# Optimization experiments

Hardware: AMD Instinct MI355X
Metric: run time of the kernel (lower is better)

Reference implementation:

```python
import jax, jax.numpy as jnp
import numpy as np

B, L, D, K, MAXL = 2, 1024, 256, 64, 1024
EPS = 1e-5

def _encode(x, pos, w1, b1, w2, b2, wa, ba):
    # x: [B,L,D] -> complex phasors [B,L,K]
    xa = x + pos[: x.shape[1]][None]
    h = jax.nn.gelu(xa @ w1 + b1, approximate=False)
    phase = jnp.tanh(h @ w2 + b2) * np.float32(np.pi)
    amp = jax.nn.softplus(xa @ wa + ba) + np.float32(0.1)
    return (amp * jnp.exp(1j * phase)).astype(jnp.complex64)

def setup_inputs() -> dict:
    key = jax.random.key(0)
    ks = jax.random.split(key, 24)
    def lin_w(k, i, o):
        return (jax.random.normal(k, (i, o), jnp.float32) / np.sqrt(np.float32(i)))
    def pos(k):
        return jax.random.normal(k, (MAXL, D), jnp.float32) * np.float32(0.02)
    inp = {
        'x': jax.random.normal(ks[0], (B, L, D), jnp.float32),
        'pos_k': pos(ks[1]),
        'w1_k': lin_w(ks[2], D, D), 'b1_k': jnp.zeros((D,), jnp.float32),
        'w2_k': lin_w(ks[3], D, K), 'b2_k': jnp.zeros((K,), jnp.float32),
        'wa_k': lin_w(ks[4], D, K), 'ba_k': jnp.zeros((K,), jnp.float32),
        'pos_q': pos(ks[5]),
        'w1_q': lin_w(ks[6], D, D), 'b1_q': jnp.zeros((D,), jnp.float32),
        'w2_q': lin_w(ks[7], D, K), 'b2_q': jnp.zeros((K,), jnp.float32),
        'wa_q': lin_w(ks[8], D, K), 'ba_q': jnp.zeros((K,), jnp.float32),
        'wv': lin_w(ks[9], D, D), 'bv': jnp.zeros((D,), jnp.float32),
        'ln_g': jnp.ones((D,), jnp.float32), 'ln_b': jnp.zeros((D,), jnp.float32),
        'wo': lin_w(ks[10], D, D), 'bo': jnp.zeros((D,), jnp.float32),
    }
    return inp

def reference(x, pos_k, w1_k, b1_k, w2_k, b2_k, wa_k, ba_k,
              pos_q, w1_q, b1_q, w2_q, b2_q, wa_q, ba_q,
              wv, bv, ln_g, ln_b, wo, bo):
    Bx, Lx, Dx = x.shape
    kp = _encode(x, pos_k, w1_k, b1_k, w2_k, b2_k, wa_k, ba_k)  # [B,L,K] complex
    qp = _encode(x, pos_q, w1_q, b1_q, w2_q, b2_q, wa_q, ba_q)  # [B,L,K] complex
    V = (x @ wv + bv).astype(jnp.complex64)                      # [B,L,D]
    bound = kp[:, :, :, None] * V[:, :, None, :]                 # [B,L,K,D]
    memory = jnp.cumsum(bound, axis=1)                           # [B,L,K,D]
    retrieved = jnp.real(jnp.einsum('blkd,blk->bld', memory, jnp.conj(qp)))
    positions = jnp.arange(1, Lx + 1, dtype=jnp.float32)
    norm = jnp.sqrt(positions * np.float32(kp.shape[-1]))[None, :, None]
    r = retrieved / norm
    mu = jnp.mean(r, axis=-1, keepdims=True)
    var = jnp.var(r, axis=-1, keepdims=True)
    rn = (r - mu) / jnp.sqrt(var + np.float32(EPS)) * ln_g + ln_b
    return x + rn @ wo + bo
```

## Files before the change

kernel.cpp:

```cpp
#include <hip/hip_runtime.h>
#include <hip/hip_bf16.h>

typedef __attribute__((ext_vector_type(8))) short short8;
typedef __attribute__((ext_vector_type(4))) float float4v;

constexpr int B = 2, L = 1024, D = 256, K = 64;
constexpr int N = B * L;
constexpr int NC = L / 64;
constexpr int TM_CSTRIDE = 2 * K * D;
constexpr int TM_BSTRIDE = NC * TM_CSTRIDE;

constexpr int WT2_OFF = 393216;

__device__ __forceinline__ ushort bf16_hi(float v) {
  return (ushort)(__float_as_uint(v) >> 16);
}
__device__ __forceinline__ float hi_f(float v) {
  return __uint_as_float(__float_as_uint(v) & 0xFFFF0000u);
}
__device__ __forceinline__ ushort bf16_rne(float v) {
  uint b = __float_as_uint(v);
  b += 0x7FFF + ((b >> 16) & 1);
  return (ushort)(b >> 16);
}

__global__ __launch_bounds__(256) void prep_kernel(
    const float* __restrict__ w1_k, const float* __restrict__ w1_q,
    const float* __restrict__ wv,
    const float* __restrict__ w2_k, const float* __restrict__ wa_k,
    const float* __restrict__ w2_q, const float* __restrict__ wa_q,
    ushort* __restrict__ WT) {
  __shared__ float Lt[64][65];
  const int bi = blockIdx.x, tid = threadIdx.x;
  const float* src;
  int ncols, k0, n0;
  ushort* dhi;
  int losz;
  if (bi < 48) {
    const int m = bi >> 4, t = bi & 15;
    src = (m == 0) ? w1_k : (m == 1) ? w1_q : wv;
    ncols = 256; k0 = (t >> 2) * 64; n0 = (t & 3) * 64;
    dhi = WT + m * 131072; losz = 65536;
  } else {
    const int m = (bi - 48) >> 2, kt = (bi - 48) & 3;
    src = (m == 0) ? w2_k : (m == 1) ? wa_k : (m == 2) ? w2_q : wa_q;
    ncols = 64; k0 = kt * 64; n0 = 0;
    dhi = WT + WT2_OFF + m * 32768; losz = 16384;
  }
  ushort* dlo = dhi + losz;
  for (int p = 0; p < 16; ++p) {
    const int kr = p * 4 + (tid >> 6), nc = tid & 63;
    Lt[kr][nc] = src[(k0 + kr) * ncols + n0 + nc];
  }
  __syncthreads();
  const int n = tid >> 2, kq = tid & 3;
  uint uh[8], ul[8];
  for (int i = 0; i < 8; ++i) {
    const float v0 = Lt[kq * 16 + 2 * i][n];
    const float v1 = Lt[kq * 16 + 2 * i + 1][n];
    uh[i] = (uint)bf16_hi(v0) | ((uint)bf16_hi(v1) << 16);
    ul[i] = (uint)bf16_rne(v0 - hi_f(v0)) | ((uint)bf16_rne(v1 - hi_f(v1)) << 16);
  }
  const int oidx = (n0 + n) * 256 + k0 + kq * 16;
  *(uint4*)&dhi[oidx] = make_uint4(uh[0], uh[1], uh[2], uh[3]);
  *(uint4*)&dhi[oidx + 8] = make_uint4(uh[4], uh[5], uh[6], uh[7]);
  *(uint4*)&dlo[oidx] = make_uint4(ul[0], ul[1], ul[2], ul[3]);
  *(uint4*)&dlo[oidx + 8] = make_uint4(ul[4], ul[5], ul[6], ul[7]);
}

__global__ __launch_bounds__(256) void enc1_kernel(
    const float* __restrict__ x, const float* __restrict__ pos_k,
    const float* __restrict__ pos_q,
    const float* __restrict__ b1_k, const float* __restrict__ b1_q,
    const float* __restrict__ bv, const ushort* __restrict__ WT,
    float* __restrict__ hk, float* __restrict__ hq, float* __restrict__ V) {
  __shared__ __align__(16) ushort Ah[32][40], Al[32][40];
  __shared__ __align__(16) ushort Bh[128][40], Bl[128][40];
  const int tid = threadIdx.x;
  const int g = blockIdx.x / 128;
  const int rem = blockIdx.x % 128;
  const int row0 = (rem >> 1) * 32, nb = (rem & 1) * 128;
  const float* pos = (g == 0) ? pos_k : (g == 1) ? pos_q : nullptr;
  const ushort* Wh = WT + g * 131072;
  const ushort* Wl = Wh + 65536;
  const int w = tid >> 6, lane = tid & 63;
  const int m16 = lane & 15, quad = lane >> 4;

  float4v acc[2][2] = {};

  for (int k0 = 0; k0 < 256; k0 += 32) {
    __syncthreads();
    {
      const int r = tid >> 3, kc = (tid & 7) * 4;
      const int row = row0 + r, l = row & (L - 1);
      float4 xv = *(const float4*)&x[row * D + k0 + kc];
      if (pos) {
        const float4 pv = *(const float4*)&pos[l * D + k0 + kc];
        xv.x += pv.x; xv.y += pv.y; xv.z += pv.z; xv.w += pv.w;
      }
      ushort4 h4, l4;
      h4.x = bf16_hi(xv.x); l4.x = bf16_rne(xv.x - hi_f(xv.x));
      h4.y = bf16_hi(xv.y); l4.y = bf16_rne(xv.y - hi_f(xv.y));
      h4.z = bf16_hi(xv.z); l4.z = bf16_rne(xv.z - hi_f(xv.z));
      h4.w = bf16_hi(xv.w); l4.w = bf16_rne(xv.w - hi_f(xv.w));
      *(ushort4*)&Ah[r][kc] = h4;
      *(ushort4*)&Al[r][kc] = l4;
    }
#pragma unroll
    for (int p = 0; p < 2; ++p) {
      const int n = (tid >> 2) + p * 64, chunk = tid & 3;
      const int ga = (nb + n) * 256 + k0 + chunk * 8;
      *(uint4*)&Bh[n][chunk * 8] = *(const uint4*)&Wh[ga];
      *(uint4*)&Bl[n][chunk * 8] = *(const uint4*)&Wl[ga];
    }
    __syncthreads();

    short8 afh[2], afl[2], bfh[2], bfl[2];
#pragma unroll
    for (int r = 0; r < 2; ++r) {
      afh[r] = *(const short8*)&Ah[r * 16 + m16][quad * 8];
      afl[r] = *(const short8*)&Al[r * 16 + m16][quad * 8];
    }
#pragma unroll
    for (int c = 0; c < 2; ++c) {
      const int col = w * 32 + c * 16 + m16;
      bfh[c] = *(const short8*)&Bh[col][quad * 8];
      bfl[c] = *(const short8*)&Bl[col][quad * 8];
    }
#pragma unroll
    for (int r = 0; r < 2; ++r)
#pragma unroll
      for (int c = 0; c < 2; ++c) {
        acc[r][c] = __builtin_amdgcn_mfma_f32_16x16x32_bf16(afh[r], bfh[c], acc[r][c], 0, 0, 0);
        acc[r][c] = __builtin_amdgcn_mfma_f32_16x16x32_bf16(afh[r], bfl[c], acc[r][c], 0, 0, 0);
        acc[r][c] = __builtin_amdgcn_mfma_f32_16x16x32_bf16(afl[r], bfh[c], acc[r][c], 0, 0, 0);
      }
  }

  float* outp = (g == 0) ? hk : (g == 1) ? hq : V;
  const float* bp = (g == 0) ? b1_k : (g == 1) ? b1_q : bv;
#pragma unroll
  for (int c = 0; c < 2; ++c) {
    const int colg = nb + w * 32 + c * 16 + m16;
    const float bias = bp[colg];
#pragma unroll
    for (int r = 0; r < 2; ++r)
#pragma unroll
      for (int j = 0; j < 4; ++j) {
        const int rowg = row0 + r * 16 + quad * 4 + j;
        float v = acc[r][c][j] + bias;
        if (g < 2) v = 0.5f * v * (1.0f + erff(v * 0.70710678f));
        outp[rowg * D + colg] = v;
      }
  }
}

__global__ __launch_bounds__(256) void enc2_kernel(
    const float* __restrict__ x, const float* __restrict__ pos_k,
    const float* __restrict__ pos_q, const float* __restrict__ hk,
    const float* __restrict__ hq,
    const float* __restrict__ b2_k, const float* __restrict__ ba_k,
    const float* __restrict__ b2_q, const float* __restrict__ ba_q,
    const ushort* __restrict__ WT,
    float* __restrict__ kr, float* __restrict__ ki,
    float* __restrict__ qr, float* __restrict__ qi) {
  __shared__ __align__(16) ushort Ahh[16][40], Ahl[16][40], Axh[16][40], Axl[16][40];
  __shared__ __align__(16) ushort B2h[64][40], B2l[64][40], Bah[64][40], Bal[64][40];
  const int tid = threadIdx.x;
  const int e = blockIdx.x >> 7;
  const int r0g = (blockIdx.x & 127) * 16;
  const float* hsrc = e ? hq : hk;
  const float* pos = e ? pos_q : pos_k;
  const ushort* W2h = WT + WT2_OFF + (e ? 2 : 0) * 32768;
  const ushort* W2l = W2h + 16384;
  const ushort* Wah = WT + WT2_OFF + (e ? 3 : 1) * 32768;
  const ushort* Wal = Wah + 16384;
  const int w = tid >> 6, lane = tid & 63;
  const int m16 = lane & 15, quad = lane >> 4;

  float4v accP = {}, accA = {};
  for (int k0 = 0; k0 < 256; k0 += 32) {
    __syncthreads();
    {
      const int r = tid >> 4, kc = (tid & 15) * 2;
      const int row = r0g + r, l = row & (L - 1);
      const float2 hv = *(const float2*)&hsrc[row * D + k0 + kc];
      const float2 xv = *(const float2*)&x[row * D + k0 + kc];
      const float2 pv = *(const float2*)&pos[l * D + k0 + kc];
      const float a0 = xv.x + pv.x, a1 = xv.y + pv.y;
      ushort2 t;
      t.x = bf16_hi(hv.x); t.y = bf16_hi(hv.y); *(ushort2*)&Ahh[r][kc] = t;
      t.x = bf16_rne(hv.x - hi_f(hv.x)); t.y = bf16_rne(hv.y - hi_f(hv.y));
      *(ushort2*)&Ahl[r][kc] = t;
      t.x = bf16_hi(a0); t.y = bf16_hi(a1); *(ushort2*)&Axh[r][kc] = t;
      t.x = bf16_rne(a0 - hi_f(a0)); t.y = bf16_rne(a1 - hi_f(a1));
      *(ushort2*)&Axl[r][kc] = t;
    }
    {
      const int n = tid >> 2, chunk = tid & 3;
      const int ga = n * 256 + k0 + chunk * 8;
      *(uint4*)&B2h[n][chunk * 8] = *(const uint4*)&W2h[ga];
      *(uint4*)&B2l[n][chunk * 8] = *(const uint4*)&W2l[ga];
      *(uint4*)&Bah[n][chunk * 8] = *(const uint4*)&Wah[ga];
      *(uint4*)&Bal[n][chunk * 8] = *(const uint4*)&Wal[ga];
    }
    __syncthreads();

    const short8 ahh = *(const short8*)&Ahh[m16][quad * 8];
    const short8 ahl = *(const short8*)&Ahl[m16][quad * 8];
    const short8 axh = *(const short8*)&Axh[m16][quad * 8];
    const short8 axl = *(const short8*)&Axl[m16][quad * 8];
    const int col = w * 16 + m16;
    const short8 b2h = *(const short8*)&B2h[col][quad * 8];
    const short8 b2l = *(const short8*)&B2l[col][quad * 8];
    const short8 bah = *(const short8*)&Bah[col][quad * 8];
    const short8 bal = *(const short8*)&Bal[col][quad * 8];
    accP = __builtin_amdgcn_mfma_f32_16x16x32_bf16(ahh, b2h, accP, 0, 0, 0);
    accP = __builtin_amdgcn_mfma_f32_16x16x32_bf16(ahh, b2l, accP, 0, 0, 0);
    accP = __builtin_amdgcn_mfma_f32_16x16x32_bf16(ahl, b2h, accP, 0, 0, 0);
    accA = __builtin_amdgcn_mfma_f32_16x16x32_bf16(axh, bah, accA, 0, 0, 0);
    accA = __builtin_amdgcn_mfma_f32_16x16x32_bf16(axh, bal, accA, 0, 0, 0);
    accA = __builtin_amdgcn_mfma_f32_16x16x32_bf16(axl, bah, accA, 0, 0, 0);
  }

  float* pr = e ? qr : kr;
  float* pim = e ? qi : ki;
  const float* b2 = e ? b2_q : b2_k;
  const float* ba = e ? ba_q : ba_k;
  const int colk = w * 16 + m16;
  const float b2v = b2[colk], bav = ba[colk];
#pragma unroll
  for (int j = 0; j < 4; ++j) {
    const int row = r0g + quad * 4 + j;
    const float ph = tanhf(accP[j] + b2v) * 3.14159265358979f;
    const float av = accA[j] + bav;
    const float am = fmaxf(av, 0.0f) + log1pf(expf(-fabsf(av))) + 0.1f;
    pr[row * K + colk] = am * cosf(ph);
    pim[row * K + colk] = am * sinf(ph);
  }
}

__global__ __launch_bounds__(256) void tbuild_kernel(
    const float* __restrict__ kr, const float* __restrict__ ki,
    const float* __restrict__ V, float* __restrict__ TM) {
  const int id = blockIdx.x;
  const int dc = id & 15, c = (id >> 4) & 15, b = id >> 8;
  const int tid = threadIdx.x;
  const int n0 = b * L + c * 64;
  const int d = dc * 16 + (tid & 15);
  const int kb = tid >> 4;

  __shared__ float krL[64][68], kiL[64][68];
  for (int e = tid; e < 1024; e += 256) {
    const int t = e >> 4, k4 = (e & 15) * 4;
    *(float4*)&krL[t][k4] = *(const float4*)&kr[(n0 + t) * K + k4];
    *(float4*)&kiL[t][k4] = *(const float4*)&ki[(n0 + t) * K + k4];
  }
  __syncthreads();

  float vcol[64];
#pragma unroll 8
  for (int t = 0; t < 64; ++t) vcol[t] = V[(n0 + t) * D + d];

  float ar[4] = {0.f, 0.f, 0.f, 0.f}, ai[4] = {0.f, 0.f, 0.f, 0.f};
#pragma unroll 4
  for (int t = 0; t < 64; ++t) {
    const float vt = vcol[t];
    const float4 k4r = *(const float4*)&krL[t][kb * 4];
    const float4 k4i = *(const float4*)&kiL[t][kb * 4];
    ar[0] += k4r.x * vt; ar[1] += k4r.y * vt; ar[2] += k4r.z * vt; ar[3] += k4r.w * vt;
    ai[0] += k4i.x * vt; ai[1] += k4i.y * vt; ai[2] += k4i.z * vt; ai[3] += k4i.w * vt;
  }

  const size_t base = (size_t)b * TM_BSTRIDE + (size_t)c * TM_CSTRIDE;
#pragma unroll
  for (int i = 0; i < 4; ++i) {
    const int k = kb * 4 + i;
    TM[base + (size_t)k * D + d] = ar[i];
    TM[base + (size_t)(K + k) * D + d] = ai[i];
  }
}

__global__ __launch_bounds__(256) void scan_kernel(float* __restrict__ TM) {
  const int col = blockIdx.x * 256 + threadIdx.x;
  const int d = col & 255;
  const int k = (col >> 8) & 63;
  const int comp = (col >> 14) & 1;
  const int b = col >> 15;
  size_t idx = (size_t)b * TM_BSTRIDE + (size_t)comp * (K * D) + (size_t)k * D + d;
  float run = 0.f;
#pragma unroll
  for (int c = 0; c < NC; ++c, idx += TM_CSTRIDE) {
    const float t = TM[idx];
    TM[idx] = run;
    run += t;
  }
}

__global__ __launch_bounds__(256) void out_kernel(
    const float* __restrict__ qr, const float* __restrict__ qi,
    const float* __restrict__ kr, const float* __restrict__ ki,
    const float* __restrict__ V, const float* __restrict__ TM,
    const float* __restrict__ x,
    const float* __restrict__ ln_g, const float* __restrict__ ln_b,
    const float* __restrict__ wo, const float* __restrict__ bo,
    float* __restrict__ out) {
  const int tid = threadIdx.x;
  const int r0 = blockIdx.x * 2;
  const int b = r0 >> 10;
  const int l0 = r0 & (L - 1);
  const int c = l0 >> 6;
  const int lo = l0 & 63;
  const int n0 = b * L + c * 64;
  const int nrows = lo + 2;

  __shared__ float qrL[2][K], qiL[2][K];
  __shared__ float krL[64][68], kiL[64][68];
  __shared__ float SL[2][64];
  __shared__ float rn[2][D];
  __shared__ float red[2][2][4];

  if (tid < 128) {
    const int r = tid >> 6, k = tid & 63;
    qrL[r][k] = qr[(r0 + r) * K + k];
    qiL[r][k] = qi[(r0 + r) * K + k];
  }
  for (int e = tid; e < nrows * 16; e += 256) {
    const int t = e >> 4, k4 = (e & 15) * 4;
    *(float4*)&krL[t][k4] = *(const float4*)&kr[(n0 + t) * K + k4];
    *(float4*)&kiL[t][k4] = *(const float4*)&ki[(n0 + t) * K + k4];
  }
  __syncthreads();

  if (tid < 128) {
    const int rq = tid >> 6, t = tid & 63;
    float s = 0.f;
    if (t <= lo + rq) {
#pragma unroll
      for (int k4 = 0; k4 < K; k4 += 4) {
        const float4 a = *(const float4*)&qrL[rq][k4];
        const float4 bb = *(const float4*)&qiL[rq][k4];
        const float4 kk = *(const float4*)&krL[t][k4];
        const float4 kki = *(const float4*)&kiL[t][k4];
        s += a.x * kk.x + a.y * kk.y + a.z * kk.z + a.w * kk.w +
             bb.x * kki.x + bb.y * kki.y + bb.z * kki.z + bb.w * kki.w;
      }
    }
    SL[rq][t] = s;
  }
  __syncthreads();

  float acc0 = 0.f, acc1 = 0.f;
  const float* Mr = TM + (size_t)b * TM_BSTRIDE + (size_t)c * TM_CSTRIDE;
  const float* Mi = Mr + K * D;
  for (int k4 = 0; k4 < K; k4 += 4) {
    const float4 q0r = *(const float4*)&qrL[0][k4];
    const float4 q0i = *(const float4*)&qiL[0][k4];
    const float4 q1r = *(const float4*)&qrL[1][k4];
    const float4 q1i = *(const float4*)&qiL[1][k4];
#pragma unroll
    for (int j = 0; j < 4; ++j) {
      const float mr = Mr[(size_t)(k4 + j) * D + tid];
      const float mi = Mi[(size_t)(k4 + j) * D + tid];
      acc0 += ((const float*)&q0r)[j] * mr + ((const float*)&q0i)[j] * mi;
      acc1 += ((const float*)&q1r)[j] * mr + ((const float*)&q1i)[j] * mi;
    }
  }
  {
    const int tmax = lo + 1;
    for (int t = 0; t <= tmax; ++t) {
      const float vt = V[(n0 + t) * D + tid];
      acc0 += SL[0][t] * vt;
      acc1 += SL[1][t] * vt;
    }
  }

  float val[2];
  val[0] = acc0 * rsqrtf((float)(l0 + 1) * 64.0f);
  val[1] = acc1 * rsqrtf((float)(l0 + 2) * 64.0f);
  const int w = tid >> 6;
#pragma unroll
  for (int rq = 0; rq < 2; ++rq) {
    float v = val[rq], v2 = v * v;
    for (int off = 32; off > 0; off >>= 1) {
      v += __shfl_xor(v, off, 64);
      v2 += __shfl_xor(v2, off, 64);
    }
    if ((tid & 63) == 0) { red[rq][0][w] = v; red[rq][1][w] = v2; }
  }
  __syncthreads();

  const float g = ln_g[tid], bb = ln_b[tid];
#pragma unroll
  for (int rq = 0; rq < 2; ++rq) {
    const float s = red[rq][0][0] + red[rq][0][1] + red[rq][0][2] + red[rq][0][3];
    const float sq = red[rq][1][0] + red[rq][1][1] + red[rq][1][2] + red[rq][1][3];
    const float mu = s * (1.0f / 256.0f);
    const float var = sq * (1.0f / 256.0f) - mu * mu;
    rn[rq][tid] = (val[rq] - mu) * rsqrtf(var + 1e-5f) * g + bb;
  }
  __syncthreads();

  float ao0, ao1;
  ao0 = ao1 = bo[tid];
  for (int d4 = 0; d4 < D; d4 += 4) {
    float wj[4];
#pragma unroll
    for (int j = 0; j < 4; ++j) wj[j] = wo[(d4 + j) * D + tid];
    const float4 r0v = *(const float4*)&rn[0][d4];
    const float4 r1v = *(const float4*)&rn[1][d4];
    ao0 += r0v.x * wj[0] + r0v.y * wj[1] + r0v.z * wj[2] + r0v.w * wj[3];
    ao1 += r1v.x * wj[0] + r1v.y * wj[1] + r1v.z * wj[2] + r1v.w * wj[3];
  }
  out[(r0 + 0) * D + tid] = x[(r0 + 0) * D + tid] + ao0;
  out[(r0 + 1) * D + tid] = x[(r0 + 1) * D + tid] + ao1;
}

extern "C" void kernel_launch(void* const* d_in, const int* in_sizes, int n_in,
                              void* d_out, int out_size, void* d_ws, size_t ws_size,
                              hipStream_t stream) {
  (void)in_sizes; (void)n_in; (void)out_size; (void)ws_size;
  const float* x    = (const float*)d_in[0];
  const float* pos_k= (const float*)d_in[1];
  const float* w1_k = (const float*)d_in[2];
  const float* b1_k = (const float*)d_in[3];
  const float* w2_k = (const float*)d_in[4];
  const float* b2_k = (const float*)d_in[5];
  const float* wa_k = (const float*)d_in[6];
  const float* ba_k = (const float*)d_in[7];
  const float* pos_q= (const float*)d_in[8];
  const float* w1_q = (const float*)d_in[9];
  const float* b1_q = (const float*)d_in[10];
  const float* w2_q = (const float*)d_in[11];
  const float* b2_q = (const float*)d_in[12];
  const float* wa_q = (const float*)d_in[13];
  const float* ba_q = (const float*)d_in[14];
  const float* wv   = (const float*)d_in[15];
  const float* bv   = (const float*)d_in[16];
  const float* ln_g = (const float*)d_in[17];
  const float* ln_b = (const float*)d_in[18];
  const float* wo   = (const float*)d_in[19];
  const float* bo   = (const float*)d_in[20];

  float* ws = (float*)d_ws;
  float* kr = ws;
  float* ki = kr + (size_t)N * K;
  float* qr = ki + (size_t)N * K;
  float* qi = qr + (size_t)N * K;
  float* V  = qi + (size_t)N * K;
  float* TM = V + (size_t)N * D;
  float* hk = TM + (size_t)B * NC * 2 * K * D;
  float* hq = hk + (size_t)N * D;
  ushort* WT = (ushort*)(hq + (size_t)N * D);

  prep_kernel<<<64, 256, 0, stream>>>(w1_k, w1_q, wv, w2_k, wa_k, w2_q, wa_q, WT);
  enc1_kernel<<<384, 256, 0, stream>>>(x, pos_k, pos_q, b1_k, b1_q, bv, WT, hk, hq, V);
  enc2_kernel<<<256, 256, 0, stream>>>(x, pos_k, pos_q, hk, hq,
                                       b2_k, ba_k, b2_q, ba_q, WT, kr, ki, qr, qi);
  tbuild_kernel<<<B * NC * 16, 256, 0, stream>>>(kr, ki, V, TM);
  scan_kernel<<<(B * 2 * K * D) / 256, 256, 0, stream>>>(TM);
  out_kernel<<<N / 2, 256, 0, stream>>>(qr, qi, kr, ki, V, TM, x,
                                        ln_g, ln_b, wo, bo, (float*)d_out);
}
```

Baseline: 165.2 us.

## Fuse weight bf16 split into encoders and process four rows per output block

Removes the separate prep kernel that pre-transposed and split weights into bf16 hi/lo pairs. The encoder GEMM kernels now read fp32 weights directly and convert them while staging into shared memory, trading one launch and a workspace round trip for redundant per-block conversion and scalar transposed LDS stores. The output kernel now handles four rows per block instead of two, using all 256 threads in the score phase, sharing TM and wo loads across more rows, and splitting accumulators for ILP.

Measured after the change: 206.4 us. 24.9% more time.

```diff
diff --git a/kernel.cpp b/kernel.cpp
--- a/kernel.cpp
+++ b/kernel.cpp
@@ -10,8 +10,6 @@
 constexpr int TM_CSTRIDE = 2 * K * D;
 constexpr int TM_BSTRIDE = NC * TM_CSTRIDE;
 
-constexpr int WT2_OFF = 393216;
-
 __device__ __forceinline__ ushort bf16_hi(float v) {
   return (ushort)(__float_as_uint(v) >> 16);
 }
@@ -24,55 +22,13 @@
   return (ushort)(b >> 16);
 }
 
-__global__ __launch_bounds__(256) void prep_kernel(
-    const float* __restrict__ w1_k, const float* __restrict__ w1_q,
-    const float* __restrict__ wv,
-    const float* __restrict__ w2_k, const float* __restrict__ wa_k,
-    const float* __restrict__ w2_q, const float* __restrict__ wa_q,
-    ushort* __restrict__ WT) {
-  __shared__ float Lt[64][65];
-  const int bi = blockIdx.x, tid = threadIdx.x;
-  const float* src;
-  int ncols, k0, n0;
-  ushort* dhi;
-  int losz;
-  if (bi < 48) {
-    const int m = bi >> 4, t = bi & 15;
-    src = (m == 0) ? w1_k : (m == 1) ? w1_q : wv;
-    ncols = 256; k0 = (t >> 2) * 64; n0 = (t & 3) * 64;
-    dhi = WT + m * 131072; losz = 65536;
-  } else {
-    const int m = (bi - 48) >> 2, kt = (bi - 48) & 3;
-    src = (m == 0) ? w2_k : (m == 1) ? wa_k : (m == 2) ? w2_q : wa_q;
-    ncols = 64; k0 = kt * 64; n0 = 0;
-    dhi = WT + WT2_OFF + m * 32768; losz = 16384;
-  }
-  ushort* dlo = dhi + losz;
-  for (int p = 0; p < 16; ++p) {
-    const int kr = p * 4 + (tid >> 6), nc = tid & 63;
-    Lt[kr][nc] = src[(k0 + kr) * ncols + n0 + nc];
-  }
-  __syncthreads();
-  const int n = tid >> 2, kq = tid & 3;
-  uint uh[8], ul[8];
-  for (int i = 0; i < 8; ++i) {
-    const float v0 = Lt[kq * 16 + 2 * i][n];
-    const float v1 = Lt[kq * 16 + 2 * i + 1][n];
-    uh[i] = (uint)bf16_hi(v0) | ((uint)bf16_hi(v1) << 16);
-    ul[i] = (uint)bf16_rne(v0 - hi_f(v0)) | ((uint)bf16_rne(v1 - hi_f(v1)) << 16);
-  }
-  const int oidx = (n0 + n) * 256 + k0 + kq * 16;
-  *(uint4*)&dhi[oidx] = make_uint4(uh[0], uh[1], uh[2], uh[3]);
-  *(uint4*)&dhi[oidx + 8] = make_uint4(uh[4], uh[5], uh[6], uh[7]);
-  *(uint4*)&dlo[oidx] = make_uint4(ul[0], ul[1], ul[2], ul[3]);
-  *(uint4*)&dlo[oidx + 8] = make_uint4(ul[4], ul[5], ul[6], ul[7]);
-}
-
 __global__ __launch_bounds__(256) void enc1_kernel(
     const float* __restrict__ x, const float* __restrict__ pos_k,
     const float* __restrict__ pos_q,
+    const float* __restrict__ w1_k, const float* __restrict__ w1_q,
+    const float* __restrict__ wv,
     const float* __restrict__ b1_k, const float* __restrict__ b1_q,
-    const float* __restrict__ bv, const ushort* __restrict__ WT,
+    const float* __restrict__ bv,
     float* __restrict__ hk, float* __restrict__ hq, float* __restrict__ V) {
   __shared__ __align__(16) ushort Ah[32][40], Al[32][40];
   __shared__ __align__(16) ushort Bh[128][40], Bl[128][40];
@@ -81,8 +37,7 @@
   const int rem = blockIdx.x % 128;
   const int row0 = (rem >> 1) * 32, nb = (rem & 1) * 128;
   const float* pos = (g == 0) ? pos_k : (g == 1) ? pos_q : nullptr;
-  const ushort* Wh = WT + g * 131072;
-  const ushort* Wl = Wh + 65536;
+  const float* Wsrc = (g == 0) ? w1_k : (g == 1) ? w1_q : wv;
   const int w = tid >> 6, lane = tid & 63;
   const int m16 = lane & 15, quad = lane >> 4;
 
@@ -106,12 +61,18 @@
       *(ushort4*)&Ah[r][kc] = h4;
       *(ushort4*)&Al[r][kc] = l4;
     }
-#pragma unroll
-    for (int p = 0; p < 2; ++p) {
-      const int n = (tid >> 2) + p * 64, chunk = tid & 3;
-      const int ga = (nb + n) * 256 + k0 + chunk * 8;
-      *(uint4*)&Bh[n][chunk * 8] = *(const uint4*)&Wh[ga];
-      *(uint4*)&Bl[n][chunk * 8] = *(const uint4*)&Wl[ga];
+    {
+      const int kk = tid >> 5;
+      const int n4 = (tid & 31) * 4;
+#pragma unroll
+      for (int p = 0; p < 4; ++p) {
+        const int kw = p * 8 + kk;
+        const float4 wv4 = *(const float4*)&Wsrc[(k0 + kw) * D + nb + n4];
+        Bh[n4 + 0][kw] = bf16_hi(wv4.x); Bl[n4 + 0][kw] = bf16_rne(wv4.x - hi_f(wv4.x));
+        Bh[n4 + 1][kw] = bf16_hi(wv4.y); Bl[n4 + 1][kw] = bf16_rne(wv4.y - hi_f(wv4.y));
+        Bh[n4 + 2][kw] = bf16_hi(wv4.z); Bl[n4 + 2][kw] = bf16_rne(wv4.z - hi_f(wv4.z));
+        Bh[n4 + 3][kw] = bf16_hi(wv4.w); Bl[n4 + 3][kw] = bf16_rne(wv4.w - hi_f(wv4.w));
+      }
     }
     __syncthreads();
 
@@ -159,9 +120,10 @@
     const float* __restrict__ x, const float* __restrict__ pos_k,
     const float* __restrict__ pos_q, const float* __restrict__ hk,
     const float* __restrict__ hq,
+    const float* __restrict__ w2_k, const float* __restrict__ wa_k,
+    const float* __restrict__ w2_q, const float* __restrict__ wa_q,
     const float* __restrict__ b2_k, const float* __restrict__ ba_k,
     const float* __restrict__ b2_q, const float* __restrict__ ba_q,
-    const ushort* __restrict__ WT,
     float* __restrict__ kr, float* __restrict__ ki,
     float* __restrict__ qr, float* __restrict__ qi) {
   __shared__ __align__(16) ushort Ahh[16][40], Ahl[16][40], Axh[16][40], Axl[16][40];
@@ -171,10 +133,8 @@
   const int r0g = (blockIdx.x & 127) * 16;
   const float* hsrc = e ? hq : hk;
   const float* pos = e ? pos_q : pos_k;
-  const ushort* W2h = WT + WT2_OFF + (e ? 2 : 0) * 32768;
-  const ushort* W2l = W2h + 16384;
-  const ushort* Wah = WT + WT2_OFF + (e ? 3 : 1) * 32768;
-  const ushort* Wal = Wah + 16384;
+  const float* W2f = e ? w2_q : w2_k;
+  const float* Waf = e ? wa_q : wa_k;
   const int w = tid >> 6, lane = tid & 63;
   const int m16 = lane & 15, quad = lane >> 4;
 
@@ -197,12 +157,15 @@
       *(ushort2*)&Axl[r][kc] = t;
     }
     {
-      const int n = tid >> 2, chunk = tid & 3;
-      const int ga = n * 256 + k0 + chunk * 8;
-      *(uint4*)&B2h[n][chunk * 8] = *(const uint4*)&W2h[ga];
-      *(uint4*)&B2l[n][chunk * 8] = *(const uint4*)&W2l[ga];
-      *(uint4*)&Bah[n][chunk * 8] = *(const uint4*)&Wah[ga];
-      *(uint4*)&Bal[n][chunk * 8] = *(const uint4*)&Wal[ga];
+      const int n = tid & 63;
+#pragma unroll
+      for (int p = 0; p < 8; ++p) {
+        const int kw = p * 4 + (tid >> 6);
+        const float v2 = W2f[(k0 + kw) * K + n];
+        const float va = Waf[(k0 + kw) * K + n];
+        B2h[n][kw] = bf16_hi(v2); B2l[n][kw] = bf16_rne(v2 - hi_f(v2));
+        Bah[n][kw] = bf16_hi(va); Bal[n][kw] = bf16_rne(va - hi_f(va));
+      }
     }
     __syncthreads();
 
@@ -306,21 +269,21 @@
     const float* __restrict__ wo, const float* __restrict__ bo,
     float* __restrict__ out) {
   const int tid = threadIdx.x;
-  const int r0 = blockIdx.x * 2;
+  const int r0 = blockIdx.x * 4;
   const int b = r0 >> 10;
   const int l0 = r0 & (L - 1);
   const int c = l0 >> 6;
   const int lo = l0 & 63;
   const int n0 = b * L + c * 64;
-  const int nrows = lo + 2;
-
-  __shared__ float qrL[2][K], qiL[2][K];
+  const int nrows = lo + 4;
+
+  __shared__ float qrL[4][K], qiL[4][K];
   __shared__ float krL[64][68], kiL[64][68];
-  __shared__ float SL[2][64];
-  __shared__ float rn[2][D];
-  __shared__ float red[2][2][4];
-
-  if (tid < 128) {
+  __shared__ float SL[4][64];
+  __shared__ float rn[4][D];
+  __shared__ float red[4][2][4];
+
+  {
     const int r = tid >> 6, k = tid & 63;
     qrL[r][k] = qr[(r0 + r) * K + k];
     qiL[r][k] = qi[(r0 + r) * K + k];
@@ -332,55 +295,68 @@
   }
   __syncthreads();
 
-  if (tid < 128) {
+  {
     const int rq = tid >> 6, t = tid & 63;
-    float s = 0.f;
+    float sA = 0.f, sB = 0.f;
     if (t <= lo + rq) {
 #pragma unroll
-      for (int k4 = 0; k4 < K; k4 += 4) {
-        const float4 a = *(const float4*)&qrL[rq][k4];
-        const float4 bb = *(const float4*)&qiL[rq][k4];
-        const float4 kk = *(const float4*)&krL[t][k4];
-        const float4 kki = *(const float4*)&kiL[t][k4];
-        s += a.x * kk.x + a.y * kk.y + a.z * kk.z + a.w * kk.w +
-             bb.x * kki.x + bb.y * kki.y + bb.z * kki.z + bb.w * kki.w;
-      }
-    }
-    SL[rq][t] = s;
+      for (int k4 = 0; k4 < K; k4 += 8) {
+        const float4 a0 = *(const float4*)&qrL[rq][k4];
+        const float4 b0 = *(const float4*)&qiL[rq][k4];
+        const float4 k0v = *(const float4*)&krL[t][k4];
+        const float4 k0i = *(const float4*)&kiL[t][k4];
+        sA += a0.x * k0v.x + a0.y * k0v.y + a0.z * k0v.z + a0.w * k0v.w +
+              b0.x * k0i.x + b0.y * k0i.y + b0.z * k0i.z + b0.w * k0i.w;
+        const float4 a1 = *(const float4*)&qrL[rq][k4 + 4];
+        const float4 b1 = *(const float4*)&qiL[rq][k4 + 4];
+        const float4 k1v = *(const float4*)&krL[t][k4 + 4];
+        const float4 k1i = *(const float4*)&kiL[t][k4 + 4];
+        sB += a1.x * k1v.x + a1.y * k1v.y + a1.z * k1v.z + a1.w * k1v.w +
+              b1.x * k1i.x + b1.y * k1i.y + b1.z * k1i.z + b1.w * k1i.w;
+      }
+    }
+    SL[rq][t] = sA + sB;
   }
   __syncthreads();
 
-  float acc0 = 0.f, acc1 = 0.f;
+  float accA[4] = {}, accB[4] = {};
   const float* Mr = TM + (size_t)b * TM_BSTRIDE + (size_t)c * TM_CSTRIDE;
   const float* Mi = Mr + K * D;
   for (int k4 = 0; k4 < K; k4 += 4) {
-    const float4 q0r = *(const float4*)&qrL[0][k4];
-    const float4 q0i = *(const float4*)&qiL[0][k4];
-    const float4 q1r = *(const float4*)&qrL[1][k4];
-    const float4 q1i = *(const float4*)&qiL[1][k4];
+    float4 q4r[4], q4i[4];
+#pragma unroll
+    for (int rq = 0; rq < 4; ++rq) {
+      q4r[rq] = *(const float4*)&qrL[rq][k4];
+      q4i[rq] = *(const float4*)&qiL[rq][k4];
+    }
 #pragma unroll
     for (int j = 0; j < 4; ++j) {
       const float mr = Mr[(size_t)(k4 + j) * D + tid];
       const float mi = Mi[(size_t)(k4 + j) * D + tid];
-      acc0 += ((const float*)&q0r)[j] * mr + ((const float*)&q0i)[j] * mi;
-      acc1 += ((const float*)&q1r)[j] * mr + ((const float*)&q1i)[j] * mi;
+      float* acc = (j & 1) ? accB : accA;
+#pragma unroll
+      for (int rq = 0; rq < 4; ++rq)
+        acc[rq] += ((const float*)&q4r[rq])[j] * mr + ((const float*)&q4i[rq])[j] * mi;
     }
   }
   {
-    const int tmax = lo + 1;
+    const int tmax = lo + 3;
+#pragma unroll 2
     for (int t = 0; t <= tmax; ++t) {
       const float vt = V[(n0 + t) * D + tid];
-      acc0 += SL[0][t] * vt;
-      acc1 += SL[1][t] * vt;
-    }
-  }
-
-  float val[2];
-  val[0] = acc0 * rsqrtf((float)(l0 + 1) * 64.0f);
-  val[1] = acc1 * rsqrtf((float)(l0 + 2) * 64.0f);
+      float* acc = (t & 1) ? accB : accA;
+#pragma unroll
+      for (int rq = 0; rq < 4; ++rq) acc[rq] += SL[rq][t] * vt;
+    }
+  }
+
+  float val[4];
+#pragma unroll
+  for (int rq = 0; rq < 4; ++rq)
+    val[rq] = (accA[rq] + accB[rq]) * rsqrtf((float)(l0 + rq + 1) * 64.0f);
   const int w = tid >> 6;
 #pragma unroll
-  for (int rq = 0; rq < 2; ++rq) {
+  for (int rq = 0; rq < 4; ++rq) {
     float v = val[rq], v2 = v * v;
     for (int off = 32; off > 0; off >>= 1) {
       v += __shfl_xor(v, off, 64);
@@ -392,7 +368,7 @@
 
   const float g = ln_g[tid], bb = ln_b[tid];
 #pragma unroll
-  for (int rq = 0; rq < 2; ++rq) {
+  for (int rq = 0; rq < 4; ++rq) {
     const float s = red[rq][0][0] + red[rq][0][1] + red[rq][0][2] + red[rq][0][3];
     const float sq = red[rq][1][0] + red[rq][1][1] + red[rq][1][2] + red[rq][1][3];
     const float mu = s * (1.0f / 256.0f);
@@ -401,19 +377,24 @@
   }
   __syncthreads();
 
-  float ao0, ao1;
-  ao0 = ao1 = bo[tid];
+  float aoA[4] = {}, aoB[4] = {};
   for (int d4 = 0; d4 < D; d4 += 4) {
     float wj[4];
 #pragma unroll
     for (int j = 0; j < 4; ++j) wj[j] = wo[(d4 + j) * D + tid];
-    const float4 r0v = *(const float4*)&rn[0][d4];
-    const float4 r1v = *(const float4*)&rn[1][d4];
-    ao0 += r0v.x * wj[0] + r0v.y * wj[1] + r0v.z * wj[2] + r0v.w * wj[3];
-    ao1 += r1v.x * wj[0] + r1v.y * wj[1] + r1v.z * wj[2] + r1v.w * wj[3];
-  }
-  out[(r0 + 0) * D + tid] = x[(r0 + 0) * D + tid] + ao0;
-  out[(r0 + 1) * D + tid] = x[(r0 + 1) * D + tid] + ao1;
+    float4 rv[4];
+#pragma unroll
+    for (int rq = 0; rq < 4; ++rq) rv[rq] = *(const float4*)&rn[rq][d4];
+#pragma unroll
+    for (int rq = 0; rq < 4; ++rq) {
+      aoA[rq] += rv[rq].x * wj[0] + rv[rq].z * wj[2];
+      aoB[rq] += rv[rq].y * wj[1] + rv[rq].w * wj[3];
+    }
+  }
+#pragma unroll
+  for (int rq = 0; rq < 4; ++rq)
+    out[(r0 + rq) * D + tid] =
+        x[(r0 + rq) * D + tid] + aoA[rq] + aoB[rq] + bo[tid];
 }
 
 extern "C" void kernel_launch(void* const* d_in, const int* in_sizes, int n_in,
@@ -451,14 +432,14 @@
   float* TM = V + (size_t)N * D;
   float* hk = TM + (size_t)B * NC * 2 * K * D;
   float* hq = hk + (size_t)N * D;
-  ushort* WT = (ushort*)(hq + (size_t)N * D);
-
-  prep_kernel<<<64, 256, 0, stream>>>(w1_k, w1_q, wv, w2_k, wa_k, w2_q, wa_q, WT);
-  enc1_kernel<<<384, 256, 0, stream>>>(x, pos_k, pos_q, b1_k, b1_q, bv, WT, hk, hq, V);
+
+  enc1_kernel<<<384, 256, 0, stream>>>(x, pos_k, pos_q, w1_k, w1_q, wv,
+                                       b1_k, b1_q, bv, hk, hq, V);
   enc2_kernel<<<256, 256, 0, stream>>>(x, pos_k, pos_q, hk, hq,
-                                       b2_k, ba_k, b2_q, ba_q, WT, kr, ki, qr, qi);
+                                       w2_k, wa_k, w2_q, wa_q,
+                                       b2_k, ba_k, b2_q, ba_q, kr, ki, qr, qi);
   tbuild_kernel<<<B * NC * 16, 256, 0, stream>>>(kr, ki, V, TM);
   scan_kernel<<<(B * 2 * K * D) / 256, 256, 0, stream>>>(TM);
-  out_kernel<<<N / 2, 256, 0, stream>>>(qr, qi, kr, ki, V, TM, x,
+  out_kernel<<<N / 4, 256, 0, stream>>>(qr, qi, kr, ki, V, TM, x,
                                         ln_g, ln_b, wo, bo, (float*)d_out);
 }
```

## Split output stage into retrieval kernel and split-bf16 MFMA output projection

Applied to the files above, without the earlier changes.

The fused output kernel is split in two. A retrieval+LayerNorm kernel now handles 4 rows per block, so each block reads the chunk memory tiles once for twice as many rows, and it writes normalized rows to workspace. A separate GEMM kernel does the wo projection with bf16 hi/lo split MFMA, using wo pre-split in the prep kernel. This removes the per-block scalar reload of the whole wo matrix, at the cost of an extra launch and a round trip of the normalized rows through global memory.

New measurement: 182.6 us. 10.5% more time.

```diff
diff --git a/kernel.cpp b/kernel.cpp
--- a/kernel.cpp
+++ b/kernel.cpp
@@ -10,7 +10,7 @@
 constexpr int TM_CSTRIDE = 2 * K * D;
 constexpr int TM_BSTRIDE = NC * TM_CSTRIDE;
 
-constexpr int WT2_OFF = 393216;
+constexpr int WT2_OFF = 524288;
 
 __device__ __forceinline__ ushort bf16_hi(float v) {
   return (ushort)(__float_as_uint(v) >> 16);
@@ -26,7 +26,7 @@
 
 __global__ __launch_bounds__(256) void prep_kernel(
     const float* __restrict__ w1_k, const float* __restrict__ w1_q,
-    const float* __restrict__ wv,
+    const float* __restrict__ wv, const float* __restrict__ wo,
     const float* __restrict__ w2_k, const float* __restrict__ wa_k,
     const float* __restrict__ w2_q, const float* __restrict__ wa_q,
     ushort* __restrict__ WT) {
@@ -36,13 +36,13 @@
   int ncols, k0, n0;
   ushort* dhi;
   int losz;
-  if (bi < 48) {
+  if (bi < 64) {
     const int m = bi >> 4, t = bi & 15;
-    src = (m == 0) ? w1_k : (m == 1) ? w1_q : wv;
+    src = (m == 0) ? w1_k : (m == 1) ? w1_q : (m == 2) ? wv : wo;
     ncols = 256; k0 = (t >> 2) * 64; n0 = (t & 3) * 64;
     dhi = WT + m * 131072; losz = 65536;
   } else {
-    const int m = (bi - 48) >> 2, kt = (bi - 48) & 3;
+    const int m = (bi - 64) >> 2, kt = (bi - 64) & 3;
     src = (m == 0) ? w2_k : (m == 1) ? wa_k : (m == 2) ? w2_q : wa_q;
     ncols = 64; k0 = kt * 64; n0 = 0;
     dhi = WT + WT2_OFF + m * 32768; losz = 16384;
@@ -297,30 +297,27 @@
   }
 }
 
-__global__ __launch_bounds__(256) void out_kernel(
+__global__ __launch_bounds__(256) void out_retr_kernel(
     const float* __restrict__ qr, const float* __restrict__ qi,
     const float* __restrict__ kr, const float* __restrict__ ki,
     const float* __restrict__ V, const float* __restrict__ TM,
-    const float* __restrict__ x,
     const float* __restrict__ ln_g, const float* __restrict__ ln_b,
-    const float* __restrict__ wo, const float* __restrict__ bo,
-    float* __restrict__ out) {
+    float* __restrict__ rnG) {
   const int tid = threadIdx.x;
-  const int r0 = blockIdx.x * 2;
+  const int r0 = blockIdx.x * 4;
   const int b = r0 >> 10;
   const int l0 = r0 & (L - 1);
   const int c = l0 >> 6;
   const int lo = l0 & 63;
   const int n0 = b * L + c * 64;
-  const int nrows = lo + 2;
-
-  __shared__ float qrL[2][K], qiL[2][K];
+  const int nrows = lo + 4;
+
+  __shared__ float qrL[4][K], qiL[4][K];
   __shared__ float krL[64][68], kiL[64][68];
-  __shared__ float SL[2][64];
-  __shared__ float rn[2][D];
-  __shared__ float red[2][2][4];
-
-  if (tid < 128) {
+  __shared__ float SL[4][64];
+  __shared__ float red[4][2][4];
+
+  {
     const int r = tid >> 6, k = tid & 63;
     qrL[r][k] = qr[(r0 + r) * K + k];
     qiL[r][k] = qi[(r0 + r) * K + k];
@@ -332,55 +329,74 @@
   }
   __syncthreads();
 
-  if (tid < 128) {
+  {
     const int rq = tid >> 6, t = tid & 63;
-    float s = 0.f;
+    float sA = 0.f, sB = 0.f;
     if (t <= lo + rq) {
 #pragma unroll
-      for (int k4 = 0; k4 < K; k4 += 4) {
-        const float4 a = *(const float4*)&qrL[rq][k4];
-        const float4 bb = *(const float4*)&qiL[rq][k4];
-        const float4 kk = *(const float4*)&krL[t][k4];
-        const float4 kki = *(const float4*)&kiL[t][k4];
-        s += a.x * kk.x + a.y * kk.y + a.z * kk.z + a.w * kk.w +
-             bb.x * kki.x + bb.y * kki.y + bb.z * kki.z + bb.w * kki.w;
+      for (int k4 = 0; k4 < K; k4 += 8) {
+        const float4 a0 = *(const float4*)&qrL[rq][k4];
+        const float4 b0 = *(const float4*)&qiL[rq][k4];
+        const float4 k0v = *(const float4*)&krL[t][k4];
+        const float4 k0i = *(const float4*)&kiL[t][k4];
+        sA += a0.x * k0v.x + a0.y * k0v.y + a0.z * k0v.z + a0.w * k0v.w +
+              b0.x * k0i.x + b0.y * k0i.y + b0.z * k0i.z + b0.w * k0i.w;
+        const float4 a1 = *(const float4*)&qrL[rq][k4 + 4];
+        const float4 b1 = *(const float4*)&qiL[rq][k4 + 4];
+        const float4 k1v = *(const float4*)&krL[t][k4 + 4];
+        const float4 k1i = *(const float4*)&kiL[t][k4 + 4];
+        sB += a1.x * k1v.x + a1.y * k1v.y + a1.z * k1v.z + a1.w * k1v.w +
+              b1.x * k1i.x + b1.y * k1i.y + b1.z * k1i.z + b1.w * k1i.w;
       }
     }
-    SL[rq][t] = s;
+    SL[rq][t] = sA + sB;
   }
   __syncthreads();
 
-  float acc0 = 0.f, acc1 = 0.f;
+  float accA[4] = {}, accB[4] = {};
   const float* Mr = TM + (size_t)b * TM_BSTRIDE + (size_t)c * TM_CSTRIDE;
   const float* Mi = Mr + K * D;
   for (int k4 = 0; k4 < K; k4 += 4) {
-    const float4 q0r = *(const float4*)&qrL[0][k4];
-    const float4 q0i = *(const float4*)&qiL[0][k4];
-    const float4 q1r = *(const float4*)&qrL[1][k4];
-    const float4 q1i = *(const float4*)&qiL[1][k4];
+    float4 q4r[4], q4i[4];
+#pragma unroll
+    for (int rq = 0; rq < 4; ++rq) {
+      q4r[rq] = *(const float4*)&qrL[rq][k4];
+      q4i[rq] = *(const float4*)&qiL[rq][k4];
+    }
+    float mr[4], mi[4];
 #pragma unroll
     for (int j = 0; j < 4; ++j) {
-      const float mr = Mr[(size_t)(k4 + j) * D + tid];
-      const float mi = Mi[(size_t)(k4 + j) * D + tid];
-      acc0 += ((const float*)&q0r)[j] * mr + ((const float*)&q0i)[j] * mi;
-      acc1 += ((const float*)&q1r)[j] * mr + ((const float*)&q1i)[j] * mi;
+      mr[j] = Mr[(size_t)(k4 + j) * D + tid];
+      mi[j] = Mi[(size_t)(k4 + j) * D + tid];
+    }
+#pragma unroll
+    for (int rq = 0; rq < 4; ++rq) {
+      accA[rq] += ((const float*)&q4r[rq])[0] * mr[0] + ((const float*)&q4i[rq])[0] * mi[0]
+                + ((const float*)&q4r[rq])[2] * mr[2] + ((const float*)&q4i[rq])[2] * mi[2];
+      accB[rq] += ((const float*)&q4r[rq])[1] * mr[1] + ((const float*)&q4i[rq])[1] * mi[1]
+                + ((const float*)&q4r[rq])[3] * mr[3] + ((const float*)&q4i[rq])[3] * mi[3];
     }
   }
   {
-    const int tmax = lo + 1;
-    for (int t = 0; t <= tmax; ++t) {
-      const float vt = V[(n0 + t) * D + tid];
-      acc0 += SL[0][t] * vt;
-      acc1 += SL[1][t] * vt;
-    }
-  }
-
-  float val[2];
-  val[0] = acc0 * rsqrtf((float)(l0 + 1) * 64.0f);
-  val[1] = acc1 * rsqrtf((float)(l0 + 2) * 64.0f);
+    const int tmax = lo + 3;
+    for (int t = 0; t < tmax; t += 2) {
+      const float vt0 = V[(n0 + t) * D + tid];
+      const float vt1 = V[(n0 + t + 1) * D + tid];
+#pragma unroll
+      for (int rq = 0; rq < 4; ++rq) {
+        accA[rq] += SL[rq][t] * vt0;
+        accB[rq] += SL[rq][t + 1] * vt1;
+      }
+    }
+  }
+
+  float val[4];
+#pragma unroll
+  for (int rq = 0; rq < 4; ++rq)
+    val[rq] = (accA[rq] + accB[rq]) * rsqrtf((float)(l0 + rq + 1) * 64.0f);
   const int w = tid >> 6;
 #pragma unroll
-  for (int rq = 0; rq < 2; ++rq) {
+  for (int rq = 0; rq < 4; ++rq) {
     float v = val[rq], v2 = v * v;
     for (int off = 32; off > 0; off >>= 1) {
       v += __shfl_xor(v, off, 64);
@@ -392,28 +408,77 @@
 
   const float g = ln_g[tid], bb = ln_b[tid];
 #pragma unroll
-  for (int rq = 0; rq < 2; ++rq) {
+  for (int rq = 0; rq < 4; ++rq) {
     const float s = red[rq][0][0] + red[rq][0][1] + red[rq][0][2] + red[rq][0][3];
     const float sq = red[rq][1][0] + red[rq][1][1] + red[rq][1][2] + red[rq][1][3];
     const float mu = s * (1.0f / 256.0f);
     const float var = sq * (1.0f / 256.0f) - mu * mu;
-    rn[rq][tid] = (val[rq] - mu) * rsqrtf(var + 1e-5f) * g + bb;
-  }
-  __syncthreads();
-
-  float ao0, ao1;
-  ao0 = ao1 = bo[tid];
-  for (int d4 = 0; d4 < D; d4 += 4) {
-    float wj[4];
-#pragma unroll
-    for (int j = 0; j < 4; ++j) wj[j] = wo[(d4 + j) * D + tid];
-    const float4 r0v = *(const float4*)&rn[0][d4];
-    const float4 r1v = *(const float4*)&rn[1][d4];
-    ao0 += r0v.x * wj[0] + r0v.y * wj[1] + r0v.z * wj[2] + r0v.w * wj[3];
-    ao1 += r1v.x * wj[0] + r1v.y * wj[1] + r1v.z * wj[2] + r1v.w * wj[3];
-  }
-  out[(r0 + 0) * D + tid] = x[(r0 + 0) * D + tid] + ao0;
-  out[(r0 + 1) * D + tid] = x[(r0 + 1) * D + tid] + ao1;
+    rnG[(r0 + rq) * D + tid] = (val[rq] - mu) * rsqrtf(var + 1e-5f) * g + bb;
+  }
+}
+
+__global__ __launch_bounds__(256) void out_gemm_kernel(
+    const float* __restrict__ rnG, const float* __restrict__ x,
+    const float* __restrict__ bo, const ushort* __restrict__ WT,
+    float* __restrict__ out) {
+  __shared__ __align__(16) ushort Ah[32][40], Al[32][40];
+  __shared__ __align__(16) ushort Bh[64][40], Bl[64][40];
+  const int tid = threadIdx.x;
+  const int row0 = (blockIdx.x >> 2) * 32, nb = (blockIdx.x & 3) * 64;
+  const ushort* Wh = WT + 3 * 131072;
+  const ushort* Wl = Wh + 65536;
+  const int w = tid >> 6, lane = tid & 63;
+  const int m16 = lane & 15, quad = lane >> 4;
+
+  float4v acc[2] = {};
+
+  for (int k0 = 0; k0 < 256; k0 += 32) {
+    __syncthreads();
+    {
+      const int r = tid >> 3, kc = (tid & 7) * 4;
+      const float4 xv = *(const float4*)&rnG[(row0 + r) * D + k0 + kc];
+      ushort4 h4, l4;
+      h4.x = bf16_hi(xv.x); l4.x = bf16_rne(xv.x - hi_f(xv.x));
+      h4.y = bf16_hi(xv.y); l4.y = bf16_rne(xv.y - hi_f(xv.y));
+      h4.z = bf16_hi(xv.z); l4.z = bf16_rne(xv.z - hi_f(xv.z));
+      h4.w = bf16_hi(xv.w); l4.w = bf16_rne(xv.w - hi_f(xv.w));
+      *(ushort4*)&Ah[r][kc] = h4;
+      *(ushort4*)&Al[r][kc] = l4;
+    }
+    {
+      const int n = tid >> 2, chunk = tid & 3;
+      const int ga = (nb + n) * 256 + k0 + chunk * 8;
+      *(uint4*)&Bh[n][chunk * 8] = *(const uint4*)&Wh[ga];
+      *(uint4*)&Bl[n][chunk * 8] = *(const uint4*)&Wl[ga];
+    }
+    __syncthreads();
+
+    short8 afh[2], afl[2];
+#pragma unroll
+    for (int r = 0; r < 2; ++r) {
+      afh[r] = *(const short8*)&Ah[r * 16 + m16][quad * 8];
+      afl[r] = *(const short8*)&Al[r * 16 + m16][quad * 8];
+    }
+    const int col = w * 16 + m16;
+    const short8 bfh = *(const short8*)&Bh[col][quad * 8];
+    const short8 bfl = *(const short8*)&Bl[col][quad * 8];
+#pragma unroll
+    for (int r = 0; r < 2; ++r) {
+      acc[r] = __builtin_amdgcn_mfma_f32_16x16x32_bf16(afh[r], bfh, acc[r], 0, 0, 0);
+      acc[r] = __builtin_amdgcn_mfma_f32_16x16x32_bf16(afh[r], bfl, acc[r], 0, 0, 0);
+      acc[r] = __builtin_amdgcn_mfma_f32_16x16x32_bf16(afl[r], bfh, acc[r], 0, 0, 0);
+    }
+  }
+
+  const int colg = nb + w * 16 + m16;
+  const float bias = bo[colg];
+#pragma unroll
+  for (int r = 0; r < 2; ++r)
+#pragma unroll
+    for (int j = 0; j < 4; ++j) {
+      const int rowg = row0 + r * 16 + quad * 4 + j;
+      out[rowg * D + colg] = x[rowg * D + colg] + acc[r][j] + bias;
+    }
 }
 
 extern "C" void kernel_launch(void* const* d_in, const int* in_sizes, int n_in,
@@ -452,13 +517,18 @@
   float* hk = TM + (size_t)B * NC * 2 * K * D;
   float* hq = hk + (size_t)N * D;
   ushort* WT = (ushort*)(hq + (size_t)N * D);
-
-  prep_kernel<<<64, 256, 0, stream>>>(w1_k, w1_q, wv, w2_k, wa_k, w2_q, wa_q, WT);
-  enc1_kernel<<<384, 256, 0, stream>>>(x, pos_k, pos_q, b1_k, b1_q, bv, WT, hk, hq, V);
+  float* rn = hk;
+
+  prep_kernel<<<80, 256, 0, stream>>>(w1_k, w1_q, wv, wo,
+                                      w2_k, wa_k, w2_q, wa_q, WT);
+  enc1_kernel<<<384, 256, 0, stream>>>(x, pos_k, pos_q, b1_k, b1_q, bv, WT,
+                                       hk, hq, V);
   enc2_kernel<<<256, 256, 0, stream>>>(x, pos_k, pos_q, hk, hq,
-                                       b2_k, ba_k, b2_q, ba_q, WT, kr, ki, qr, qi);
+                                       b2_k, ba_k, b2_q, ba_q, WT,
+                                       kr, ki, qr, qi);
   tbuild_kernel<<<B * NC * 16, 256, 0, stream>>>(kr, ki, V, TM);
   scan_kernel<<<(B * 2 * K * D) / 256, 256, 0, stream>>>(TM);
-  out_kernel<<<N / 2, 256, 0, stream>>>(qr, qi, kr, ki, V, TM, x,
-                                        ln_g, ln_b, wo, bo, (float*)d_out);
-}
+  out_retr_kernel<<<N / 4, 256, 0, stream>>>(qr, qi, kr, ki, V, TM,
+                                             ln_g, ln_b, rn);
+  out_gemm_kernel<<<256, 256, 0, stream>>>(rn, x, bo, WT, (float*)d_out);
+}
```
